# Performance work log

Hardware: AMD Instinct MI355X
Metric: run time of the kernel (lower is better)

The kernel has to match this reference:

```python
import jax, jax.numpy as jnp
import numpy as np

B, D, H = 8192, 1024, 1024


def setup_inputs() -> dict:
    key = jax.random.key(0)
    k = jax.random.split(key, 6)
    s_x = 1.0 / np.sqrt(D)
    s_h = 1.0 / np.sqrt(H)
    return {
        "x": jax.random.normal(k[0], (B, D), dtype=jnp.float32),
        "h_prev": jax.random.normal(k[1], (B, H), dtype=jnp.float32),
        "c_prev": jax.random.normal(k[2], (B, H), dtype=jnp.float32),
        # Stacked gate weights in order [i, f, o, g] (exactly equivalent to
        # the 8 separate nn.Linear layers, fused into 2 GEMMs).
        "Wx": jax.random.uniform(k[3], (4 * H, D), jnp.float32, -s_x, s_x),
        "Wh": jax.random.uniform(k[4], (4 * H, H), jnp.float32, -s_h, s_h),
        # combined bias of W_* and U_* linears per gate
        "b": jax.random.uniform(k[5], (4 * H,), jnp.float32, -s_x, s_x),
    }


def reference(x, h_prev, c_prev, Wx, Wh, b):
    # gates: [B, 4H], gate order i, f, o, g
    gates = x @ Wx.T + h_prev @ Wh.T + b
    i, f, o, g = jnp.split(gates, 4, axis=-1)
    c_t = jax.nn.sigmoid(f) * c_prev + jax.nn.sigmoid(i) * jnp.tanh(g)
    h_t = jax.nn.sigmoid(o) * jnp.tanh(c_t)
    return (h_t, c_t)
```

## Files before the change

### kernel.cpp

```cpp
#include <hip/hip_runtime.h>
#include <hip/hip_bf16.h>
#include <stdint.h>

#define B_ROWS 8192
#define D_DIM  1024
#define H_DIM  1024
#define K_DIM  2048

#define BM 128
#define BN 64
#define BK 64

typedef __bf16 bf16x8 __attribute__((ext_vector_type(8)));
typedef float  f32x4  __attribute__((ext_vector_type(4)));

__device__ __forceinline__ float sigm(float x) {
  return 1.0f / (1.0f + __expf(-x));
}
__device__ __forceinline__ float tanh_fast(float x) {
  return 1.0f - 2.0f / (__expf(2.0f * x) + 1.0f);
}

__device__ __forceinline__ int sw(int row, int chunk) {
  return row * BK + ((chunk ^ (row & 7)) << 3);
}

__global__ __launch_bounds__(256, 2) void lstm_f32(
    const float* __restrict__ x, const float* __restrict__ h_prev,
    const float* __restrict__ c_prev, const float* __restrict__ Wx,
    const float* __restrict__ Wh, const float* __restrict__ bias,
    float* __restrict__ h_out, float* __restrict__ c_out) {
  __shared__ __hip_bfloat16 sA[BM * BK];
  __shared__ __hip_bfloat16 sB[4 * BN * BK];

  const int tid  = threadIdx.x;
  const int wave = tid >> 6;
  const int lane = tid & 63;
  const int m0 = blockIdx.x * BM;
  const int n0 = blockIdx.y * BN;

  const int wm = wave >> 1, wn = wave & 1;
  const int lr = lane & 15, quad = lane >> 4;

  f32x4 acc[4][4][2];
#pragma unroll
  for (int g = 0; g < 4; ++g)
#pragma unroll
    for (int ti = 0; ti < 4; ++ti)
#pragma unroll
      for (int tj = 0; tj < 2; ++tj) {
        f32x4 z = {0.0f, 0.0f, 0.0f, 0.0f};
        acc[g][ti][tj] = z;
      }

  const int srow = lane >> 3;
  const int lc   = lane & 7;
  const int scol = lc << 3;

  for (int k0 = 0; k0 < K_DIM; k0 += BK) {
    const float* aSrc; const float* wSrc; int kh;
    if (k0 < D_DIM) { aSrc = x;      wSrc = Wx; kh = k0; }
    else            { aSrc = h_prev; wSrc = Wh; kh = k0 - D_DIM; }

    f32x4 stg[12][2];
#pragma unroll
    for (int t = 0; t < 12; ++t) {
      const int chunk = wave + t * 4;
      const float* g;
      if (chunk < 16) {
        const int row = chunk * 8 + srow;
        g = aSrc + (size_t)(m0 + row) * 1024 + kh + scol;
      } else {
        const int j = chunk - 16;
        const int gate = j >> 3;
        const int row = (j & 7) * 8 + srow;
        g = wSrc + (size_t)(gate * H_DIM + n0 + row) * 1024 + kh + scol;
      }
      stg[t][0] = *(const f32x4*)g;
      stg[t][1] = *(const f32x4*)(g + 4);
    }

    __syncthreads();

#pragma unroll
    for (int t = 0; t < 12; ++t) {
      const int chunk = wave + t * 4;
      bf16x8 v;
#pragma unroll
      for (int i = 0; i < 4; ++i) {
        v[i]     = (__bf16)stg[t][0][i];
        v[i + 4] = (__bf16)stg[t][1][i];
      }
      __hip_bfloat16* dst;
      if (chunk < 16) {
        const int row = chunk * 8 + srow;
        dst = &sA[sw(row, lc)];
      } else {
        const int j = chunk - 16;
        const int row = (j & 7) * 8 + srow;
        dst = &sB[(j >> 3) * (BN * BK) + sw(row, lc)];
      }
      *(bf16x8*)dst = v;
    }
    __syncthreads();

#pragma unroll
    for (int kk = 0; kk < BK; kk += 32) {
      const int cbase = kk >> 3;
      bf16x8 af[4];
#pragma unroll
      for (int ti = 0; ti < 4; ++ti)
        af[ti] = *(const bf16x8*)&sA[sw(wm * 64 + ti * 16 + lr, cbase + quad)];
      bf16x8 bw[4][2];
#pragma unroll
      for (int g = 0; g < 4; ++g)
#pragma unroll
        for (int tj = 0; tj < 2; ++tj)
          bw[g][tj] = *(const bf16x8*)
              &sB[g * (BN * BK) + sw(wn * 32 + tj * 16 + lr, cbase + quad)];
#pragma unroll
      for (int g = 0; g < 4; ++g)
#pragma unroll
        for (int ti = 0; ti < 4; ++ti)
#pragma unroll
          for (int tj = 0; tj < 2; ++tj)
            acc[g][ti][tj] = __builtin_amdgcn_mfma_f32_16x16x32_bf16(
                af[ti], bw[g][tj], acc[g][ti][tj], 0, 0, 0);
    }
  }

  const size_t TOT = (size_t)B_ROWS * H_DIM;
#pragma unroll
  for (int tj = 0; tj < 2; ++tj) {
    const int n = n0 + wn * 32 + tj * 16 + lr;
    const float bi = bias[n];
    const float bf = bias[H_DIM + n];
    const float bo = bias[2 * H_DIM + n];
    const float bg = bias[3 * H_DIM + n];
#pragma unroll
    for (int ti = 0; ti < 4; ++ti) {
#pragma unroll
      for (int r = 0; r < 4; ++r) {
        const int m = m0 + wm * 64 + ti * 16 + quad * 4 + r;
        const size_t off = (size_t)m * H_DIM + n;
        const float iv = acc[0][ti][tj][r] + bi;
        const float fv = acc[1][ti][tj][r] + bf;
        const float ov = acc[2][ti][tj][r] + bo;
        const float gv = acc[3][ti][tj][r] + bg;
        const float cp = c_prev[off];
        const float ct = sigm(fv) * cp + sigm(iv) * tanh_fast(gv);
        const float ht = sigm(ov) * tanh_fast(ct);
        h_out[off] = ht;
        c_out[off] = ct;
      }
    }
  }
}

extern "C" void kernel_launch(void* const* d_in, const int* in_sizes, int n_in,
                              void* d_out, int out_size, void* d_ws, size_t ws_size,
                              hipStream_t stream) {
  const float* x      = (const float*)d_in[0];
  const float* h_prev = (const float*)d_in[1];
  const float* c_prev = (const float*)d_in[2];
  const float* Wx     = (const float*)d_in[3];
  const float* Wh     = (const float*)d_in[4];
  const float* b      = (const float*)d_in[5];
  float* h_out = (float*)d_out;
  float* c_out = (float*)d_out + (size_t)B_ROWS * H_DIM;

  dim3 grid(B_ROWS / BM, H_DIM / BN, 1);
  lstm_f32<<<grid, 256, 0, stream>>>(x, h_prev, c_prev, Wx, Wh, b, h_out, c_out);
}
```

Before: 367.0 us.

## Pre-pack operands to bf16 MFMA tiles and stream them with global_load_lds

Adds a pre-pass kernel that converts x, h_prev, Wx and Wh to bf16 and stores them in a workspace as 16x32 tiles already ordered for the MFMA fragments. The GEMM kernel then copies these tiles straight into LDS with async global-to-LDS loads, so the per-block fp32 load, convert and swizzled store is gone and global reads are halved. The cost is an extra kernel launch plus a full write and reread of the packed operands through HBM each call. LDS reads are now unswizzled contiguous fragments. The old fp32 kernel is kept as a fallback when the workspace is too small.

```diff
diff --git a/kernel.cpp b/kernel.cpp
--- a/kernel.cpp
+++ b/kernel.cpp
@@ -6,13 +6,23 @@
 #define D_DIM  1024
 #define H_DIM  1024
 #define K_DIM  2048
+#define N_GATES 4096
 
 #define BM 128
 #define BN 64
 #define BK 64
 
+#define KC (K_DIM / 32)
+#define A_M16 (B_ROWS / 16)
+#define W_N16 (N_GATES / 16)
+#define A_CHUNKS (A_M16 * KC)
+#define W_CHUNKS (W_N16 * KC)
+#define A_WS_BYTES ((size_t)A_CHUNKS * 1024)
+#define W_WS_BYTES ((size_t)W_CHUNKS * 1024)
+
 typedef __bf16 bf16x8 __attribute__((ext_vector_type(8)));
 typedef float  f32x4  __attribute__((ext_vector_type(4)));
+using bf16_t = __hip_bfloat16;
 
 __device__ __forceinline__ float sigm(float x) {
   return 1.0f / (1.0f + __expf(-x));
@@ -21,17 +31,52 @@
   return 1.0f - 2.0f / (__expf(2.0f * x) + 1.0f);
 }
 
-__device__ __forceinline__ int sw(int row, int chunk) {
-  return row * BK + ((chunk ^ (row & 7)) << 3);
-}
-
-__global__ __launch_bounds__(256, 2) void lstm_f32(
-    const float* __restrict__ x, const float* __restrict__ h_prev,
-    const float* __restrict__ c_prev, const float* __restrict__ Wx,
-    const float* __restrict__ Wh, const float* __restrict__ bias,
+__device__ __forceinline__ void async_ld16(const void* g, void* l) {
+  __builtin_amdgcn_global_load_lds(
+      (const __attribute__((address_space(1))) unsigned int*)g,
+      (__attribute__((address_space(3))) unsigned int*)l, 16, 0, 0);
+}
+
+__global__ void pack_tiles(const float* __restrict__ x,
+                           const float* __restrict__ h,
+                           const float* __restrict__ Wx,
+                           const float* __restrict__ Wh,
+                           bf16_t* __restrict__ aws,
+                           bf16_t* __restrict__ wws) {
+  const int wave = threadIdx.x >> 6, lane = threadIdx.x & 63;
+  int c = blockIdx.x * 4 + wave;
+  const int r16 = lane & 15, quad = lane >> 4;
+  const float* src;
+  size_t soff;
+  bf16_t* dst;
+  if (c < A_CHUNKS) {
+    const int m16 = c / KC, k32 = c % KC;
+    const int k = k32 * 32 + quad * 8;
+    src = (k < D_DIM) ? x : h;
+    soff = (size_t)(m16 * 16 + r16) * 1024 + (k & 1023);
+    dst = aws + (size_t)c * 512;
+  } else {
+    c -= A_CHUNKS;
+    const int n16 = c / KC, k32 = c % KC;
+    const int k = k32 * 32 + quad * 8;
+    src = (k < D_DIM) ? Wx : Wh;
+    soff = (size_t)(n16 * 16 + r16) * 1024 + (k & 1023);
+    dst = wws + (size_t)c * 512;
+  }
+  const f32x4 a = *(const f32x4*)(src + soff);
+  const f32x4 b = *(const f32x4*)(src + soff + 4);
+  bf16x8 v;
+#pragma unroll
+  for (int i = 0; i < 4; ++i) { v[i] = (__bf16)a[i]; v[i + 4] = (__bf16)b[i]; }
+  *(bf16x8*)(dst + lane * 8) = v;
+}
+
+__global__ __launch_bounds__(256, 2) void lstm_mfma(
+    const bf16_t* __restrict__ aws, const bf16_t* __restrict__ wws,
+    const float* __restrict__ c_prev, const float* __restrict__ bias,
     float* __restrict__ h_out, float* __restrict__ c_out) {
-  __shared__ __hip_bfloat16 sA[BM * BK];
-  __shared__ __hip_bfloat16 sB[4 * BN * BK];
+  __shared__ bf16_t sA[16 * 512];
+  __shared__ bf16_t sB[32 * 512];
 
   const int tid  = threadIdx.x;
   const int wave = tid >> 6;
@@ -41,6 +86,8 @@
 
   const int wm = wave >> 1, wn = wave & 1;
   const int lr = lane & 15, quad = lane >> 4;
+  const int m16_0 = m0 >> 4;
+  const int n16_0 = n0 >> 4;
 
   f32x4 acc[4][4][2];
 #pragma unroll
@@ -53,71 +100,43 @@
         acc[g][ti][tj] = z;
       }
 
-  const int srow = lane >> 3;
-  const int lc   = lane & 7;
-  const int scol = lc << 3;
-
   for (int k0 = 0; k0 < K_DIM; k0 += BK) {
-    const float* aSrc; const float* wSrc; int kh;
-    if (k0 < D_DIM) { aSrc = x;      wSrc = Wx; kh = k0; }
-    else            { aSrc = h_prev; wSrc = Wh; kh = k0 - D_DIM; }
-
-    f32x4 stg[12][2];
+    const int kq0 = k0 >> 5;
+
+    __syncthreads();
 #pragma unroll
     for (int t = 0; t < 12; ++t) {
-      const int chunk = wave + t * 4;
-      const float* g;
-      if (chunk < 16) {
-        const int row = chunk * 8 + srow;
-        g = aSrc + (size_t)(m0 + row) * 1024 + kh + scol;
+      const int ch = t * 4 + wave;
+      const bf16_t* g;
+      bf16_t* l;
+      if (ch < 16) {
+        const int mi = ch >> 1, kq = ch & 1;
+        g = aws + ((size_t)(m16_0 + mi) * KC + kq0 + kq) * 512;
+        l = sA + ch * 512;
       } else {
-        const int j = chunk - 16;
-        const int gate = j >> 3;
-        const int row = (j & 7) * 8 + srow;
-        g = wSrc + (size_t)(gate * H_DIM + n0 + row) * 1024 + kh + scol;
-      }
-      stg[t][0] = *(const f32x4*)g;
-      stg[t][1] = *(const f32x4*)(g + 4);
-    }
-
+        const int j = ch - 16;
+        const int ni = j >> 1, kq = j & 1;
+        const int n16 = (ni >> 2) * (H_DIM / 16) + n16_0 + (ni & 3);
+        g = wws + ((size_t)n16 * KC + kq0 + kq) * 512;
+        l = sB + j * 512;
+      }
+      async_ld16(g + lane * 8, l + lane * 8);
+    }
     __syncthreads();
 
 #pragma unroll
-    for (int t = 0; t < 12; ++t) {
-      const int chunk = wave + t * 4;
-      bf16x8 v;
-#pragma unroll
-      for (int i = 0; i < 4; ++i) {
-        v[i]     = (__bf16)stg[t][0][i];
-        v[i + 4] = (__bf16)stg[t][1][i];
-      }
-      __hip_bfloat16* dst;
-      if (chunk < 16) {
-        const int row = chunk * 8 + srow;
-        dst = &sA[sw(row, lc)];
-      } else {
-        const int j = chunk - 16;
-        const int row = (j & 7) * 8 + srow;
-        dst = &sB[(j >> 3) * (BN * BK) + sw(row, lc)];
-      }
-      *(bf16x8*)dst = v;
-    }
-    __syncthreads();
-
-#pragma unroll
-    for (int kk = 0; kk < BK; kk += 32) {
-      const int cbase = kk >> 3;
+    for (int kq = 0; kq < 2; ++kq) {
       bf16x8 af[4];
 #pragma unroll
       for (int ti = 0; ti < 4; ++ti)
-        af[ti] = *(const bf16x8*)&sA[sw(wm * 64 + ti * 16 + lr, cbase + quad)];
+        af[ti] = *(const bf16x8*)&sA[((wm * 4 + ti) * 2 + kq) * 512 + lane * 8];
       bf16x8 bw[4][2];
 #pragma unroll
       for (int g = 0; g < 4; ++g)
 #pragma unroll
         for (int tj = 0; tj < 2; ++tj)
           bw[g][tj] = *(const bf16x8*)
-              &sB[g * (BN * BK) + sw(wn * 32 + tj * 16 + lr, cbase + quad)];
+              &sB[((g * 4 + wn * 2 + tj) * 2 + kq) * 512 + lane * 8];
 #pragma unroll
       for (int g = 0; g < 4; ++g)
 #pragma unroll
@@ -157,6 +176,117 @@
   }
 }
 
+__device__ __forceinline__ int sw_(int row, int chunk) {
+  return row * BK + ((chunk ^ (row & 7)) << 3);
+}
+
+__global__ __launch_bounds__(256, 2) void lstm_f32(
+    const float* __restrict__ x, const float* __restrict__ h_prev,
+    const float* __restrict__ c_prev, const float* __restrict__ Wx,
+    const float* __restrict__ Wh, const float* __restrict__ bias,
+    float* __restrict__ h_out, float* __restrict__ c_out) {
+  __shared__ bf16_t sA[BM * BK];
+  __shared__ bf16_t sB[4 * BN * BK];
+  const int tid = threadIdx.x, wave = tid >> 6, lane = tid & 63;
+  const int m0 = blockIdx.x * BM, n0 = blockIdx.y * BN;
+  const int wm = wave >> 1, wn = wave & 1;
+  const int lr = lane & 15, quad = lane >> 4;
+  f32x4 acc[4][4][2];
+#pragma unroll
+  for (int g = 0; g < 4; ++g)
+#pragma unroll
+    for (int ti = 0; ti < 4; ++ti)
+#pragma unroll
+      for (int tj = 0; tj < 2; ++tj) {
+        f32x4 z = {0.0f, 0.0f, 0.0f, 0.0f};
+        acc[g][ti][tj] = z;
+      }
+  const int srow = lane >> 3, lc = lane & 7, scol = lc << 3;
+  for (int k0 = 0; k0 < K_DIM; k0 += BK) {
+    const float* aSrc; const float* wSrc; int kh;
+    if (k0 < D_DIM) { aSrc = x; wSrc = Wx; kh = k0; }
+    else            { aSrc = h_prev; wSrc = Wh; kh = k0 - D_DIM; }
+    f32x4 stg[12][2];
+#pragma unroll
+    for (int t = 0; t < 12; ++t) {
+      const int chunk = wave + t * 4;
+      const float* g;
+      if (chunk < 16) {
+        g = aSrc + (size_t)(m0 + chunk * 8 + srow) * 1024 + kh + scol;
+      } else {
+        const int j = chunk - 16;
+        g = wSrc + (size_t)((j >> 3) * H_DIM + n0 + (j & 7) * 8 + srow) * 1024 + kh + scol;
+      }
+      stg[t][0] = *(const f32x4*)g;
+      stg[t][1] = *(const f32x4*)(g + 4);
+    }
+    __syncthreads();
+#pragma unroll
+    for (int t = 0; t < 12; ++t) {
+      const int chunk = wave + t * 4;
+      bf16x8 v;
+#pragma unroll
+      for (int i = 0; i < 4; ++i) {
+        v[i] = (__bf16)stg[t][0][i];
+        v[i + 4] = (__bf16)stg[t][1][i];
+      }
+      bf16_t* dst;
+      if (chunk < 16) dst = &sA[sw_(chunk * 8 + srow, lc)];
+      else {
+        const int j = chunk - 16;
+        dst = &sB[(j >> 3) * (BN * BK) + sw_((j & 7) * 8 + srow, lc)];
+      }
+      *(bf16x8*)dst = v;
+    }
+    __syncthreads();
+#pragma unroll
+    for (int kk = 0; kk < BK; kk += 32) {
+      const int cbase = kk >> 3;
+      bf16x8 af[4];
+#pragma unroll
+      for (int ti = 0; ti < 4; ++ti)
+        af[ti] = *(const bf16x8*)&sA[sw_(wm * 64 + ti * 16 + lr, cbase + quad)];
+      bf16x8 bw[4][2];
+#pragma unroll
+      for (int g = 0; g < 4; ++g)
+#pragma unroll
+        for (int tj = 0; tj < 2; ++tj)
+          bw[g][tj] = *(const bf16x8*)
+              &sB[g * (BN * BK) + sw_(wn * 32 + tj * 16 + lr, cbase + quad)];
+#pragma unroll
+      for (int g = 0; g < 4; ++g)
+#pragma unroll
+        for (int ti = 0; ti < 4; ++ti)
+#pragma unroll
+          for (int tj = 0; tj < 2; ++tj)
+            acc[g][ti][tj] = __builtin_amdgcn_mfma_f32_16x16x32_bf16(
+                af[ti], bw[g][tj], acc[g][ti][tj], 0, 0, 0);
+    }
+  }
+  const size_t TOT = (size_t)B_ROWS * H_DIM;
+#pragma unroll
+  for (int tj = 0; tj < 2; ++tj) {
+    const int n = n0 + wn * 32 + tj * 16 + lr;
+    const float bi = bias[n], bf = bias[H_DIM + n];
+    const float bo = bias[2 * H_DIM + n], bg = bias[3 * H_DIM + n];
+#pragma unroll
+    for (int ti = 0; ti < 4; ++ti)
+#pragma unroll
+      for (int r = 0; r < 4; ++r) {
+        const int m = m0 + wm * 64 + ti * 16 + quad * 4 + r;
+        const size_t off = (size_t)m * H_DIM + n;
+        const float iv = acc[0][ti][tj][r] + bi;
+        const float fv = acc[1][ti][tj][r] + bf;
+        const float ov = acc[2][ti][tj][r] + bo;
+        const float gv = acc[3][ti][tj][r] + bg;
+        const float cp = c_prev[off];
+        const float ct = sigm(fv) * cp + sigm(iv) * tanh_fast(gv);
+        h_out[off] = sigm(ov) * tanh_fast(ct);
+        c_out[off] = ct;
+      }
+  }
+}
+
 extern "C" void kernel_launch(void* const* d_in, const int* in_sizes, int n_in,
                               void* d_out, int out_size, void* d_ws, size_t ws_size,
                               hipStream_t stream) {
@@ -170,5 +300,13 @@
   float* c_out = (float*)d_out + (size_t)B_ROWS * H_DIM;
 
   dim3 grid(B_ROWS / BM, H_DIM / BN, 1);
-  lstm_f32<<<grid, 256, 0, stream>>>(x, h_prev, c_prev, Wx, Wh, b, h_out, c_out);
-}
+  if (ws_size >= A_WS_BYTES + W_WS_BYTES) {
+    bf16_t* aws = (bf16_t*)d_ws;
+    bf16_t* wws = (bf16_t*)((char*)d_ws + A_WS_BYTES);
+    pack_tiles<<<(A_CHUNKS + W_CHUNKS) / 4, 256, 0, stream>>>(x, h_prev, Wx, Wh,
+                                                              aws, wws);
+    lstm_mfma<<<grid, 256, 0, stream>>>(aws, wws, c_prev, b, h_out, c_out);
+  } else {
+    lstm_f32<<<grid, 256, 0, stream>>>(x, h_prev, c_prev, Wx, Wh, b, h_out, c_out);
+  }
+}
```

Measured after the change: 312.8 us. -14.8%, faster.
